# Performance work log

Hardware: AMD Instinct MI355X
Metric: run time of the kernel (lower is better)

## Reference

```python
import jax, jax.numpy as jnp
import numpy as np

# MLS-MPM constants (init_kwargs)
N_GRID = 128
DT = 2e-4
DX = 1.0 / N_GRID
INV_DX = float(N_GRID)
P_VOL = (DX * 0.5) ** 3
P_RHO = 1000.0
P_MASS = P_VOL * P_RHO
GRAVITY = 9.8
BOUND = 3
N_PART = 500_000

# 27 neighbor offsets for quadratic B-spline stencil
_OFFS = np.stack(np.meshgrid(np.arange(3), np.arange(3), np.arange(3), indexing='ij'), -1).reshape(27, 3)


def setup_inputs() -> dict:
    key = jax.random.key(0)
    k1, k2, k3, k4, k5 = jax.random.split(key, 5)
    # particles strictly inside the domain, away from boundary cells
    x = 0.2 + 0.6 * jax.random.uniform(k1, (N_PART, 3), dtype=jnp.float32)
    v = 0.1 * jax.random.normal(k2, (N_PART, 3), dtype=jnp.float32)
    C = 0.1 * jax.random.normal(k3, (N_PART, 3, 3), dtype=jnp.float32)
    F = jnp.eye(3, dtype=jnp.float32) + 0.01 * jax.random.normal(k4, (N_PART, 3, 3), dtype=jnp.float32)
    stress = 1e2 * jax.random.normal(k5, (N_PART, 3, 3), dtype=jnp.float32)
    return {"x": x, "v": v, "C": C, "F": F, "stress": stress}


def _mpm_step(x, v, C, F, stress):
    dtype = x.dtype
    base = jnp.floor(x * INV_DX - 0.5).astype(jnp.int32)          # [N,3]
    fx = x * INV_DX - base.astype(dtype)                          # [N,3] in [0.5, 1.5)
    # quadratic B-spline weights per node offset (0,1,2) per axis: [N,3off,3ax]
    w = jnp.stack([0.5 * (1.5 - fx) ** 2,
                   0.75 - (fx - 1.0) ** 2,
                   0.5 * (fx - 0.5) ** 2], axis=1)
    offs = jnp.asarray(_OFFS, dtype=jnp.int32)                    # [27,3]
    weight = w[:, offs[:, 0], 0] * w[:, offs[:, 1], 1] * w[:, offs[:, 2], 2]  # [N,27]
    dpos = (offs[None].astype(dtype) - fx[:, None, :]) * DX       # [N,27,3] world units

    # P2G scatter: momentum (3) + mass (1) per grid node
    affine = (-DT * P_VOL * 4.0 * INV_DX * INV_DX) * stress + P_MASS * C   # [N,3,3]
    mv = P_MASS * v[:, None, :] + jnp.einsum('nij,nkj->nki', affine, dpos) # [N,27,3]
    vals = jnp.concatenate([weight[..., None] * mv,
                            (weight * P_MASS)[..., None]], axis=-1)        # [N,27,4]
    node = jnp.clip(base[:, None, :] + offs[None], 0, N_GRID - 1)          # [N,27,3]
    flat = (node[..., 0] * N_GRID + node[..., 1]) * N_GRID + node[..., 2]  # [N,27]
    grid = jnp.zeros((N_GRID ** 3, 4), dtype).at[flat.reshape(-1)].add(vals.reshape(-1, 4))

    # grid update: normalize momentum, gravity, sticky boundary
    gm = grid[:, 3:4]
    occ = gm[:, 0] > 0
    gv = jnp.where(gm > 0, grid[:, :3] / jnp.maximum(gm, 1e-10), 0.0)
    gv = gv.at[:, 1].add(jnp.where(occ, jnp.asarray(-DT * GRAVITY, dtype), 0.0))
    gv3 = gv.reshape(N_GRID, N_GRID, N_GRID, 3)
    idx = jnp.arange(N_GRID)
    for axis in range(3):  # fixed 3-axis loop (not a data loop)
        shp = [1, 1, 1]; shp[axis] = N_GRID
        lo = (idx < BOUND).reshape(shp)
        hi = (idx >= N_GRID - BOUND).reshape(shp)
        comp = gv3[..., axis]
        comp = jnp.where(lo & (comp < 0), 0.0, comp)
        comp = jnp.where(hi & (comp > 0), 0.0, comp)
        gv3 = gv3.at[..., axis].set(comp)
    gvf = gv3.reshape(-1, 3)

    # G2P gather
    gvp = gvf[flat]                                               # [N,27,3]
    v_next = jnp.einsum('nk,nkd->nd', weight, gvp)
    C_next = (4.0 * INV_DX * INV_DX) * jnp.einsum('nk,nki,nkj->nij', weight, gvp, dpos)
    x_next = x + DT * v_next
    F_next = jnp.einsum('nij,njk->nik', jnp.eye(3, dtype=dtype) + DT * C_next, F)
    return x_next, v_next, C_next, F_next


def reference(x, v, C, F, stress):
    return _mpm_step(x, v, C, F, stress)
```

## Files before the change

kernel.cpp:

```cpp
#include <hip/hip_runtime.h>
#include <limits.h>

#define N_GRID 128
#define N_GRID3 (N_GRID * N_GRID * N_GRID)

constexpr int   N_PART   = 500000;
constexpr float DT       = 0.0002f;
constexpr float DX       = 1.0f / 128.0f;
constexpr float INV_DX   = 128.0f;
constexpr float P_MASS   = 5.9604644775390625e-05f;
constexpr float AFF_COEF = -7.8125e-07f;
constexpr float GRAVITY  = 9.8f;
constexpr int   BOUND    = 3;
constexpr float C_SCALE  = 65536.0f;
constexpr int   ZQ       = 2;

__global__ __launch_bounds__(256) void k_count(const float* __restrict__ x,
                                               int* __restrict__ cnt,
                                               int* __restrict__ blkMin,
                                               int* __restrict__ blkMax) {
  __shared__ int lmin[12], lmax[12];
  int n = blockIdx.x * 256 + threadIdx.x;
  int bx = INT_MAX, by = INT_MAX, bz = INT_MAX;
  int mx = -1, my = -1, mz = -1;
  if (n < N_PART) {
    bx = min(max((int)floorf(x[n * 3 + 0] * INV_DX - 0.5f), 0), N_GRID - 1);
    by = min(max((int)floorf(x[n * 3 + 1] * INV_DX - 0.5f), 0), N_GRID - 1);
    bz = min(max((int)floorf(x[n * 3 + 2] * INV_DX - 0.5f), 0), N_GRID - 1);
    int c = (bx << 14) | (by << 7) | bz;
    atomicAdd(&cnt[c], 1);
    mx = bx; my = by; mz = bz;
  }
#pragma unroll
  for (int d = 32; d > 0; d >>= 1) {
    bx = min(bx, __shfl_xor(bx, d));
    by = min(by, __shfl_xor(by, d));
    bz = min(bz, __shfl_xor(bz, d));
    mx = max(mx, __shfl_xor(mx, d));
    my = max(my, __shfl_xor(my, d));
    mz = max(mz, __shfl_xor(mz, d));
  }
  int lane = threadIdx.x & 63, wid = threadIdx.x >> 6;
  if (lane == 0) {
    lmin[wid * 3 + 0] = bx; lmin[wid * 3 + 1] = by; lmin[wid * 3 + 2] = bz;
    lmax[wid * 3 + 0] = mx; lmax[wid * 3 + 1] = my; lmax[wid * 3 + 2] = mz;
  }
  __syncthreads();
  if (threadIdx.x == 0) {
    int b = blockIdx.x;
#pragma unroll
    for (int a = 0; a < 3; ++a) {
      blkMin[b * 3 + a] = min(min(lmin[a], lmin[3 + a]), min(lmin[6 + a], lmin[9 + a]));
      blkMax[b * 3 + a] = max(max(lmax[a], lmax[3 + a]), max(lmax[6 + a], lmax[9 + a]));
    }
  }
}

__global__ __launch_bounds__(256) void k_scan1(const int* __restrict__ cnt,
                                               int* __restrict__ blkSum) {
  __shared__ int ws[4];
  int tid = threadIdx.x, lane = tid & 63, wid = tid >> 6;
  int4 v = ((const int4*)cnt)[blockIdx.x * 256 + tid];
  int s = v.x + v.y + v.z + v.w;
  for (int d = 32; d > 0; d >>= 1) s += __shfl_down(s, d);
  if (lane == 0) ws[wid] = s;
  __syncthreads();
  if (tid == 0) blkSum[blockIdx.x] = ws[0] + ws[1] + ws[2] + ws[3];
}

__global__ __launch_bounds__(256) void k_scan2(const int* __restrict__ blkSum,
                                               int* __restrict__ blkOff,
                                               int* __restrict__ start,
                                               const int* __restrict__ blkMin,
                                               const int* __restrict__ blkMax,
                                               int nblkP,
                                               int* __restrict__ bbox) {
  __shared__ int wsum[4];
  __shared__ int rmin[12], rmax[12];
  int tid = threadIdx.x, lane = tid & 63, wid = tid >> 6;

  int base = tid * 8;
  int s[8], tot = 0;
#pragma unroll
  for (int j = 0; j < 8; ++j) { s[j] = blkSum[base + j]; tot += s[j]; }
  int incl = tot;
  for (int d = 1; d < 64; d <<= 1) {
    int t = __shfl_up(incl, d);
    if (lane >= d) incl += t;
  }
  if (lane == 63) wsum[wid] = incl;
  __syncthreads();
  int woff = 0;
  for (int w = 0; w < wid; ++w) woff += wsum[w];
  int run = woff + incl - tot;
#pragma unroll
  for (int j = 0; j < 8; ++j) { blkOff[base + j] = run; run += s[j]; }
  if (tid == 255) start[N_GRID3] = run;

  int bx = INT_MAX, by = INT_MAX, bz = INT_MAX;
  int mx = -1, my = -1, mz = -1;
  for (int j = tid; j < nblkP; j += 256) {
    bx = min(bx, blkMin[j * 3 + 0]);
    by = min(by, blkMin[j * 3 + 1]);
    bz = min(bz, blkMin[j * 3 + 2]);
    mx = max(mx, blkMax[j * 3 + 0]);
    my = max(my, blkMax[j * 3 + 1]);
    mz = max(mz, blkMax[j * 3 + 2]);
  }
#pragma unroll
  for (int d = 32; d > 0; d >>= 1) {
    bx = min(bx, __shfl_xor(bx, d));
    by = min(by, __shfl_xor(by, d));
    bz = min(bz, __shfl_xor(bz, d));
    mx = max(mx, __shfl_xor(mx, d));
    my = max(my, __shfl_xor(my, d));
    mz = max(mz, __shfl_xor(mz, d));
  }
  if (lane == 0) {
    rmin[wid * 3 + 0] = bx; rmin[wid * 3 + 1] = by; rmin[wid * 3 + 2] = bz;
    rmax[wid * 3 + 0] = mx; rmax[wid * 3 + 1] = my; rmax[wid * 3 + 2] = mz;
  }
  __syncthreads();
  if (tid == 0) {
#pragma unroll
    for (int a = 0; a < 3; ++a) {
      bbox[a]     = min(min(rmin[a], rmin[3 + a]), min(rmin[6 + a], rmin[9 + a]));
      bbox[3 + a] = max(max(rmax[a], rmax[3 + a]), max(rmax[6 + a], rmax[9 + a]));
    }
  }
}

__global__ __launch_bounds__(256) void k_scan3(int* __restrict__ cnt,
                                               const int* __restrict__ blkOff,
                                               int* __restrict__ start) {
  __shared__ int wsum[4];
  int tid = threadIdx.x, lane = tid & 63, wid = tid >> 6;
  int b = blockIdx.x;
  int4 v = ((const int4*)cnt)[b * 256 + tid];
  int s = v.x + v.y + v.z + v.w;
  int incl = s;
  for (int d = 1; d < 64; d <<= 1) {
    int t = __shfl_up(incl, d);
    if (lane >= d) incl += t;
  }
  if (lane == 63) wsum[wid] = incl;
  __syncthreads();
  int woff = blkOff[b];
  for (int w = 0; w < wid; ++w) woff += wsum[w];
  int run = woff + incl - s;
  int i0 = (b * 256 + tid) * 4;
  int r0 = run, r1 = r0 + v.x, r2 = r1 + v.y, r3 = r2 + v.z;
  start[i0 + 0] = r0; start[i0 + 1] = r1; start[i0 + 2] = r2; start[i0 + 3] = r3;
  cnt[i0 + 0] = r0; cnt[i0 + 1] = r1; cnt[i0 + 2] = r2; cnt[i0 + 3] = r3;
}

__global__ __launch_bounds__(256) void k_reorder(
    const float* __restrict__ x, const float* __restrict__ v,
    const float* __restrict__ C, const float* __restrict__ S,
    int* __restrict__ cursor, float4* __restrict__ posO,
    float4* __restrict__ aux) {
  int n = blockIdx.x * 256 + threadIdx.x;
  if (n >= N_PART) return;

  float px = x[n * 3 + 0], py = x[n * 3 + 1], pz = x[n * 3 + 2];
  int bx = min(max((int)floorf(px * INV_DX - 0.5f), 0), N_GRID - 1);
  int by = min(max((int)floorf(py * INV_DX - 0.5f), 0), N_GRID - 1);
  int bz = min(max((int)floorf(pz * INV_DX - 0.5f), 0), N_GRID - 1);
  int c = (bx << 14) | (by << 7) | bz;
  int pos = atomicAdd(&cursor[c], 1);

  float mvx = P_MASS * v[n * 3 + 0];
  float mvy = P_MASS * v[n * 3 + 1];
  float mvz = P_MASS * v[n * 3 + 2];
  float aff[9];
#pragma unroll
  for (int k = 0; k < 9; ++k)
    aff[k] = AFF_COEF * S[n * 9 + k] + P_MASS * C[n * 9 + k];

  posO[pos] = make_float4(px, py, pz, __int_as_float(n));
  float4* dst = aux + (size_t)pos * 3;
  dst[0] = make_float4(mvx, mvy, mvz, aff[0]);
  dst[1] = make_float4(aff[1], aff[2], aff[3], aff[4]);
  dst[2] = make_float4(aff[5], aff[6], aff[7], aff[8]);
}

__device__ __forceinline__ float wq(int o, float f) {
  if (o == 0) return 0.5f * (1.5f - f) * (1.5f - f);
  if (o == 1) return 0.75f - (f - 1.0f) * (f - 1.0f);
  return 0.5f * (f - 0.5f) * (f - 0.5f);
}

__global__ __launch_bounds__(256) void mpm_p2g(
    const int* __restrict__ start, const float4* __restrict__ posO,
    const float4* __restrict__ aux, const int* __restrict__ bbox,
    float* __restrict__ grid ) {
  int bx0 = bbox[0], by0 = bbox[1], bz0c = bbox[2];
  int nxd = bbox[3] - bx0 + 3;
  int nyd = bbox[4] - by0 + 3;
  int nzd = bbox[5] - bz0c + 3;
  int dimzq = (nzd + ZQ - 1) / ZQ;
  int vol = nxd * nyd * dimzq;
  int nact = (vol + 255) >> 8;

  int bid = blockIdx.x;
  if (bid >= nact) return;
  int q = nact >> 3, r = nact & 7;
  int xcd = bid & 7, sub = bid >> 3;
  int wgid = (xcd < r ? xcd * (q + 1) : r * (q + 1) + (xcd - r) * q) + sub;

  int t = wgid * 256 + (int)threadIdx.x;
  if (t >= vol) return;
  int izq = t % dimzq;
  int rr = t / dimzq;
  int iy = rr % nyd;
  int ix = rr / nyd;
  int nx = bx0 + ix, ny = by0 + iy, nz0 = bz0c + izq * ZQ;
  if (nx > N_GRID - 1 || ny > N_GRID - 1) return;
  int zb0 = nz0 - 2;
  bool zint = (zb0 >= 0) && (zb0 + ZQ + 2 <= N_GRID);

  float accx[ZQ], accy[ZQ], accz[ZQ], accm[ZQ];
#pragma unroll
  for (int k = 0; k < ZQ; ++k) { accx[k] = 0.f; accy[k] = 0.f; accz[k] = 0.f; accm[k] = 0.f; }
  int gotmask = 0;

#pragma unroll
  for (int dy = -2; dy <= 0; ++dy) {
    int cy = ny + dy;
    if (cy < 0) continue;
#pragma unroll
    for (int dx = -2; dx <= 0; ++dx) {
      int cx = nx + dx;
      if (cx < 0) continue;
      const int ox = -dx, oy = -dy;
      int rowb = (cx << 14) | (cy << 7);

      int S[ZQ + 3];
      if (zint) {
#pragma unroll
        for (int j = 0; j < ZQ + 3; ++j) S[j] = start[rowb + zb0 + j];
      } else {
#pragma unroll
        for (int j = 0; j < ZQ + 3; ++j)
          S[j] = start[rowb + min(max(zb0 + j, 0), N_GRID)];
      }
#pragma unroll
      for (int k = 0; k < ZQ; ++k)
        gotmask |= (S[k + 3] > S[k]) ? (1 << k) : 0;

      for (int i = S[0]; i < S[ZQ + 2]; ++i) {
        float4 q0 = posO[i];
        const float4* ap = aux + (size_t)i * 3;
        float4 A0 = ap[0], A1 = ap[1], A2 = ap[2];

        float fx = q0.x * INV_DX - (float)cx;
        float fy = q0.y * INV_DX - (float)cy;
        float gz = q0.z * INV_DX;
        float bzf = floorf(gz - 0.5f);
        float fz = gz - bzf;
        int oz0 = nz0 - (int)bzf;

        float wxy = wq(ox, fx) * wq(oy, fy);
        float dpx = ((float)ox - fx) * DX;
        float dpy = ((float)oy - fy) * DX;
        float wz0 = 0.5f * (1.5f - fz) * (1.5f - fz);
        float wz1 = 0.75f - (fz - 1.0f) * (fz - 1.0f);
        float wz2 = 0.5f * (fz - 0.5f) * (fz - 0.5f);

        float sx = A0.x + A0.w * dpx + A1.x * dpy;
        float sy = A0.y + A1.z * dpx + A1.w * dpy;
        float sz = A0.z + A2.y * dpx + A2.z * dpy;
        float wm = wxy * P_MASS;

#pragma unroll
        for (int k = 0; k < ZQ; ++k) {
          int oz = oz0 + k;
          if (oz < 0 || oz > 2) continue;
          float wzz = (oz == 0) ? wz0 : ((oz == 1) ? wz1 : wz2);
          float w = wxy * wzz;
          float dpz = ((float)oz - fz) * DX;
          accx[k] += w * (sx + A1.y * dpz);
          accy[k] += w * (sy + A2.x * dpz);
          accz[k] += w * (sz + A2.w * dpz);
          accm[k] += wzz * wm;
        }
      }
    }
  }

  if (!gotmask) return;

  float4* g4 = (float4*)grid;
#pragma unroll
  for (int k = 0; k < ZQ; ++k) {
    int nz = nz0 + k;
    if (!((gotmask >> k) & 1) || nz > N_GRID - 1) continue;
    float m = accm[k];
    float ovx = 0.0f, ovy = 0.0f, ovz = 0.0f;
    if (m > 0.0f) {
      float inv = 1.0f / fmaxf(m, 1e-10f);
      ovx = accx[k] * inv;
      ovy = accy[k] * inv;
      ovz = accz[k] * inv;
      ovy -= DT * GRAVITY;
    }
    if (nx < BOUND && ovx < 0.0f) ovx = 0.0f;
    if (nx >= N_GRID - BOUND && ovx > 0.0f) ovx = 0.0f;
    if (ny < BOUND && ovy < 0.0f) ovy = 0.0f;
    if (ny >= N_GRID - BOUND && ovy > 0.0f) ovy = 0.0f;
    if (nz < BOUND && ovz < 0.0f) ovz = 0.0f;
    if (nz >= N_GRID - BOUND && ovz > 0.0f) ovz = 0.0f;
    g4[(nx << 14) | (ny << 7) | nz] = make_float4(ovx, ovy, ovz, m);
  }
}

__global__ __launch_bounds__(256) void mpm_g2p(
    const float4* __restrict__ posO, const float* __restrict__ grid,
    float* __restrict__ out_x, float* __restrict__ out_v,
    float* __restrict__ out_C) {
  int i = blockIdx.x * blockDim.x + threadIdx.x;
  if (i >= N_PART) return;

  float4 q0 = posO[i];
  int n = __float_as_int(q0.w);

  float px = q0.x, py = q0.y, pz = q0.z;
  float gx = px * INV_DX, gy = py * INV_DX, gz = pz * INV_DX;
  int bx = (int)floorf(gx - 0.5f);
  int by = (int)floorf(gy - 0.5f);
  int bz = (int)floorf(gz - 0.5f);
  float fx = gx - (float)bx, fy = gy - (float)by, fz = gz - (float)bz;

  float wx[3], wy[3], wz[3];
  wx[0] = 0.5f * (1.5f - fx) * (1.5f - fx);
  wx[1] = 0.75f - (fx - 1.0f) * (fx - 1.0f);
  wx[2] = 0.5f * (fx - 0.5f) * (fx - 0.5f);
  wy[0] = 0.5f * (1.5f - fy) * (1.5f - fy);
  wy[1] = 0.75f - (fy - 1.0f) * (fy - 1.0f);
  wy[2] = 0.5f * (fy - 0.5f) * (fy - 0.5f);
  wz[0] = 0.5f * (1.5f - fz) * (1.5f - fz);
  wz[1] = 0.75f - (fz - 1.0f) * (fz - 1.0f);
  wz[2] = 0.5f * (fz - 0.5f) * (fz - 0.5f);

  float vnx = 0.0f, vny = 0.0f, vnz = 0.0f;
  float Cn[9];
#pragma unroll
  for (int k = 0; k < 9; ++k) Cn[k] = 0.0f;

  const float4* g4 = (const float4*)grid;
  bool interior = (bx >= 0) & (by >= 0) & (bz >= 0) &
                  (bx + 2 < N_GRID) & (by + 2 < N_GRID) & (bz + 2 < N_GRID);

  if (interior) {
    int flat0 = (bx << 14) | (by << 7) | bz;
#pragma unroll
    for (int a = 0; a < 3; ++a) {
#pragma unroll
      for (int bb = 0; bb < 3; ++bb) {
#pragma unroll
        for (int c = 0; c < 3; ++c) {
          float weight = wx[a] * wy[bb] * wz[c];
          float dpx = ((float)a - fx) * DX;
          float dpy = ((float)bb - fy) * DX;
          float dpz = ((float)c - fz) * DX;
          float4 g = g4[flat0 + (a << 14) + (bb << 7) + c];
          vnx += weight * g.x;
          vny += weight * g.y;
          vnz += weight * g.z;
          Cn[0] += weight * g.x * dpx;
          Cn[1] += weight * g.x * dpy;
          Cn[2] += weight * g.x * dpz;
          Cn[3] += weight * g.y * dpx;
          Cn[4] += weight * g.y * dpy;
          Cn[5] += weight * g.y * dpz;
          Cn[6] += weight * g.z * dpx;
          Cn[7] += weight * g.z * dpy;
          Cn[8] += weight * g.z * dpz;
        }
      }
    }
  } else {
#pragma unroll
    for (int a = 0; a < 3; ++a) {
#pragma unroll
      for (int bb = 0; bb < 3; ++bb) {
#pragma unroll
        for (int c = 0; c < 3; ++c) {
          float weight = wx[a] * wy[bb] * wz[c];
          float dpx = ((float)a - fx) * DX;
          float dpy = ((float)bb - fy) * DX;
          float dpz = ((float)c - fz) * DX;
          int nxg = min(max(bx + a, 0), N_GRID - 1);
          int nyg = min(max(by + bb, 0), N_GRID - 1);
          int nzg = min(max(bz + c, 0), N_GRID - 1);
          float4 g = g4[(nxg << 14) | (nyg << 7) | nzg];
          vnx += weight * g.x;
          vny += weight * g.y;
          vnz += weight * g.z;
          Cn[0] += weight * g.x * dpx;
          Cn[1] += weight * g.x * dpy;
          Cn[2] += weight * g.x * dpz;
          Cn[3] += weight * g.y * dpx;
          Cn[4] += weight * g.y * dpy;
          Cn[5] += weight * g.y * dpz;
          Cn[6] += weight * g.z * dpx;
          Cn[7] += weight * g.z * dpy;
          Cn[8] += weight * g.z * dpz;
        }
      }
    }
  }

#pragma unroll
  for (int k = 0; k < 9; ++k) Cn[k] *= C_SCALE;

  out_x[n * 3 + 0] = px + DT * vnx;
  out_x[n * 3 + 1] = py + DT * vny;
  out_x[n * 3 + 2] = pz + DT * vnz;
  out_v[n * 3 + 0] = vnx;
  out_v[n * 3 + 1] = vny;
  out_v[n * 3 + 2] = vnz;
#pragma unroll
  for (int k = 0; k < 9; ++k) out_C[n * 9 + k] = Cn[k];
}

__global__ __launch_bounds__(256) void k_ffinal(
    const float* __restrict__ out_C, const float* __restrict__ F,
    float* __restrict__ out_F) {
  int n = blockIdx.x * blockDim.x + threadIdx.x;
  if (n >= N_PART) return;

  float A[9];
#pragma unroll
  for (int k = 0; k < 9; ++k) A[k] = DT * out_C[(size_t)n * 9 + k];
  A[0] += 1.0f; A[4] += 1.0f; A[8] += 1.0f;

  float Fl[9];
#pragma unroll
  for (int k = 0; k < 9; ++k) Fl[k] = F[(size_t)n * 9 + k];

#pragma unroll
  for (int r = 0; r < 3; ++r) {
#pragma unroll
    for (int k = 0; k < 3; ++k) {
      float s = A[r * 3 + 0] * Fl[0 * 3 + k] +
                A[r * 3 + 1] * Fl[1 * 3 + k] +
                A[r * 3 + 2] * Fl[2 * 3 + k];
      out_F[(size_t)n * 9 + r * 3 + k] = s;
    }
  }
}

extern "C" void kernel_launch(void* const* d_in, const int* in_sizes, int n_in,
                              void* d_out, int out_size, void* d_ws, size_t ws_size,
                              hipStream_t stream) {
  const float* x      = (const float*)d_in[0];
  const float* v      = (const float*)d_in[1];
  const float* C      = (const float*)d_in[2];
  const float* F      = (const float*)d_in[3];
  const float* stress = (const float*)d_in[4];

  float* out = (float*)d_out;
  char*  ws  = (char*)d_ws;

  const size_t GRID_BYTES  = (size_t)N_GRID3 * 4 * sizeof(float);
  const size_t POSO_BYTES  = (size_t)N_PART * sizeof(float4);
  const size_t AUX_BYTES   = (size_t)N_PART * 3 * sizeof(float4);
  const size_t CNT_BYTES   = (size_t)N_GRID3 * sizeof(int);
  const size_t START_BYTES = ((size_t)N_GRID3 + 1) * sizeof(int);

  int pblocks = (N_PART + 255) / 256;

  size_t off = 0;
  float*  grid   = (float*)(ws + off);  off += GRID_BYTES;
  float4* posO   = (float4*)(ws + off); off += POSO_BYTES;
  float4* aux    = (float4*)(ws + off); off += AUX_BYTES;
  int*    cnt    = (int*)(ws + off);    off += CNT_BYTES;
  int*    startp = (int*)(ws + off);    off += START_BYTES;
  int*    blkSum = (int*)(ws + off);    off += 2048 * sizeof(int);
  int*    blkOff = (int*)(ws + off);    off += 2048 * sizeof(int);
  int*    blkMin = (int*)(ws + off);    off += (size_t)pblocks * 3 * sizeof(int);
  int*    blkMax = (int*)(ws + off);    off += (size_t)pblocks * 3 * sizeof(int);
  int*    bbox   = (int*)(ws + off);    off += 16 * sizeof(int);

  hipMemsetAsync(cnt, 0, CNT_BYTES, stream);

  k_count<<<pblocks, 256, 0, stream>>>(x, cnt, blkMin, blkMax);
  k_scan1<<<2048, 256, 0, stream>>>(cnt, blkSum);
  k_scan2<<<1, 256, 0, stream>>>(blkSum, blkOff, startp, blkMin, blkMax, pblocks, bbox);
  k_scan3<<<2048, 256, 0, stream>>>(cnt, blkOff, startp);
  k_reorder<<<pblocks, 256, 0, stream>>>(x, v, C, stress, cnt, posO, aux);

  mpm_p2g<<<(N_GRID3 / ZQ + 255) / 256, 256, 0, stream>>>(startp, posO, aux, bbox, grid);

  float* out_x = out;
  float* out_v = out + (size_t)N_PART * 3;
  float* out_C = out + (size_t)N_PART * 6;
  float* out_F = out + (size_t)N_PART * 6 + (size_t)N_PART * 9;
  mpm_g2p<<<pblocks, 256, 0, stream>>>(posO, grid, out_x, out_v, out_C);
  k_ffinal<<<pblocks, 256, 0, stream>>>(out_C, F, out_F);
}
```

Baseline: 189.7 us.

## Split reorder into permutation and gather kernels with interleaved 64-byte payload

The fused reorder kernel, which scattered 64 bytes per particle to random sorted positions, is split in two. One kernel writes only a permutation index, and a second kernel gathers each particle's inputs in sorted order and writes them coalesced. Position and affine data are merged into one 64-byte record per particle, so P2G reads a single contiguous line per particle. This adds an extra launch and random-gather reads of the inputs, and G2P now reads with a 64-byte stride.

```diff
diff --git a/kernel.cpp b/kernel.cpp
--- a/kernel.cpp
+++ b/kernel.cpp
@@ -154,21 +154,29 @@
   cnt[i0 + 0] = r0; cnt[i0 + 1] = r1; cnt[i0 + 2] = r2; cnt[i0 + 3] = r3;
 }
 
-__global__ __launch_bounds__(256) void k_reorder(
+__global__ __launch_bounds__(256) void k_perm(const float* __restrict__ x,
+                                              int* __restrict__ cursor,
+                                              int* __restrict__ perm) {
+  int n = blockIdx.x * 256 + threadIdx.x;
+  if (n >= N_PART) return;
+  int bx = min(max((int)floorf(x[n * 3 + 0] * INV_DX - 0.5f), 0), N_GRID - 1);
+  int by = min(max((int)floorf(x[n * 3 + 1] * INV_DX - 0.5f), 0), N_GRID - 1);
+  int bz = min(max((int)floorf(x[n * 3 + 2] * INV_DX - 0.5f), 0), N_GRID - 1);
+  int c = (bx << 14) | (by << 7) | bz;
+  int pos = atomicAdd(&cursor[c], 1);
+  perm[pos] = n;
+}
+
+__global__ __launch_bounds__(256) void k_gather(
+    const int* __restrict__ perm,
     const float* __restrict__ x, const float* __restrict__ v,
     const float* __restrict__ C, const float* __restrict__ S,
-    int* __restrict__ cursor, float4* __restrict__ posO,
-    float4* __restrict__ aux) {
-  int n = blockIdx.x * 256 + threadIdx.x;
-  if (n >= N_PART) return;
+    float4* __restrict__ pay) {
+  int pos = blockIdx.x * 256 + threadIdx.x;
+  if (pos >= N_PART) return;
+  int n = perm[pos];
 
   float px = x[n * 3 + 0], py = x[n * 3 + 1], pz = x[n * 3 + 2];
-  int bx = min(max((int)floorf(px * INV_DX - 0.5f), 0), N_GRID - 1);
-  int by = min(max((int)floorf(py * INV_DX - 0.5f), 0), N_GRID - 1);
-  int bz = min(max((int)floorf(pz * INV_DX - 0.5f), 0), N_GRID - 1);
-  int c = (bx << 14) | (by << 7) | bz;
-  int pos = atomicAdd(&cursor[c], 1);
-
   float mvx = P_MASS * v[n * 3 + 0];
   float mvy = P_MASS * v[n * 3 + 1];
   float mvz = P_MASS * v[n * 3 + 2];
@@ -177,11 +185,11 @@
   for (int k = 0; k < 9; ++k)
     aff[k] = AFF_COEF * S[n * 9 + k] + P_MASS * C[n * 9 + k];
 
-  posO[pos] = make_float4(px, py, pz, __int_as_float(n));
-  float4* dst = aux + (size_t)pos * 3;
-  dst[0] = make_float4(mvx, mvy, mvz, aff[0]);
-  dst[1] = make_float4(aff[1], aff[2], aff[3], aff[4]);
-  dst[2] = make_float4(aff[5], aff[6], aff[7], aff[8]);
+  float4* dst = pay + (size_t)pos * 4;
+  dst[0] = make_float4(px, py, pz, __int_as_float(n));
+  dst[1] = make_float4(mvx, mvy, mvz, aff[0]);
+  dst[2] = make_float4(aff[1], aff[2], aff[3], aff[4]);
+  dst[3] = make_float4(aff[5], aff[6], aff[7], aff[8]);
 }
 
 __device__ __forceinline__ float wq(int o, float f) {
@@ -191,8 +199,8 @@
 }
 
 __global__ __launch_bounds__(256) void mpm_p2g(
-    const int* __restrict__ start, const float4* __restrict__ posO,
-    const float4* __restrict__ aux, const int* __restrict__ bbox,
+    const int* __restrict__ start, const float4* __restrict__ pay,
+    const int* __restrict__ bbox,
     float* __restrict__ grid ) {
   int bx0 = bbox[0], by0 = bbox[1], bz0c = bbox[2];
   int nxd = bbox[3] - bx0 + 3;
@@ -249,9 +257,8 @@
         gotmask |= (S[k + 3] > S[k]) ? (1 << k) : 0;
 
       for (int i = S[0]; i < S[ZQ + 2]; ++i) {
-        float4 q0 = posO[i];
-        const float4* ap = aux + (size_t)i * 3;
-        float4 A0 = ap[0], A1 = ap[1], A2 = ap[2];
+        const float4* src = pay + (size_t)i * 4;
+        float4 q0 = src[0], A0 = src[1], A1 = src[2], A2 = src[3];
 
         float fx = q0.x * INV_DX - (float)cx;
         float fy = q0.y * INV_DX - (float)cy;
@@ -315,13 +322,13 @@
 }
 
 __global__ __launch_bounds__(256) void mpm_g2p(
-    const float4* __restrict__ posO, const float* __restrict__ grid,
+    const float4* __restrict__ pay, const float* __restrict__ grid,
     float* __restrict__ out_x, float* __restrict__ out_v,
     float* __restrict__ out_C) {
   int i = blockIdx.x * blockDim.x + threadIdx.x;
   if (i >= N_PART) return;
 
-  float4 q0 = posO[i];
+  float4 q0 = pay[(size_t)i * 4];
   int n = __float_as_int(q0.w);
 
   float px = q0.x, py = q0.y, pz = q0.z;
@@ -464,19 +471,19 @@
   char*  ws  = (char*)d_ws;
 
   const size_t GRID_BYTES  = (size_t)N_GRID3 * 4 * sizeof(float);
-  const size_t POSO_BYTES  = (size_t)N_PART * sizeof(float4);
-  const size_t AUX_BYTES   = (size_t)N_PART * 3 * sizeof(float4);
+  const size_t PAY_BYTES   = (size_t)N_PART * 4 * sizeof(float4);
   const size_t CNT_BYTES   = (size_t)N_GRID3 * sizeof(int);
   const size_t START_BYTES = ((size_t)N_GRID3 + 1) * sizeof(int);
+  const size_t PERM_BYTES  = (size_t)N_PART * sizeof(int);
 
   int pblocks = (N_PART + 255) / 256;
 
   size_t off = 0;
   float*  grid   = (float*)(ws + off);  off += GRID_BYTES;
-  float4* posO   = (float4*)(ws + off); off += POSO_BYTES;
-  float4* aux    = (float4*)(ws + off); off += AUX_BYTES;
+  float4* pay    = (float4*)(ws + off); off += PAY_BYTES;
   int*    cnt    = (int*)(ws + off);    off += CNT_BYTES;
   int*    startp = (int*)(ws + off);    off += START_BYTES;
+  int*    perm   = (int*)(ws + off);    off += PERM_BYTES;
   int*    blkSum = (int*)(ws + off);    off += 2048 * sizeof(int);
   int*    blkOff = (int*)(ws + off);    off += 2048 * sizeof(int);
   int*    blkMin = (int*)(ws + off);    off += (size_t)pblocks * 3 * sizeof(int);
@@ -489,14 +496,15 @@
   k_scan1<<<2048, 256, 0, stream>>>(cnt, blkSum);
   k_scan2<<<1, 256, 0, stream>>>(blkSum, blkOff, startp, blkMin, blkMax, pblocks, bbox);
   k_scan3<<<2048, 256, 0, stream>>>(cnt, blkOff, startp);
-  k_reorder<<<pblocks, 256, 0, stream>>>(x, v, C, stress, cnt, posO, aux);
-
-  mpm_p2g<<<(N_GRID3 / ZQ + 255) / 256, 256, 0, stream>>>(startp, posO, aux, bbox, grid);
+  k_perm<<<pblocks, 256, 0, stream>>>(x, cnt, perm);
+  k_gather<<<pblocks, 256, 0, stream>>>(perm, x, v, C, stress, pay);
+
+  mpm_p2g<<<(N_GRID3 / ZQ + 255) / 256, 256, 0, stream>>>(startp, pay, bbox, grid);
 
   float* out_x = out;
   float* out_v = out + (size_t)N_PART * 3;
   float* out_C = out + (size_t)N_PART * 6;
   float* out_F = out + (size_t)N_PART * 6 + (size_t)N_PART * 9;
-  mpm_g2p<<<pblocks, 256, 0, stream>>>(posO, grid, out_x, out_v, out_C);
+  mpm_g2p<<<pblocks, 256, 0, stream>>>(pay, grid, out_x, out_v, out_C);
   k_ffinal<<<pblocks, 256, 0, stream>>>(out_C, F, out_F);
 }
```

After: 239.0 us. 26.0% more time.
